# Kernel tuning notes

Hardware: AMD Instinct MI355X
Metric: run time of the kernel (lower is better)

## Reference

```python
import jax, jax.numpy as jnp
import numpy as np
from jax import lax

K = 3  # kernel_size
PAD = K // 2

def setup_inputs() -> dict:
    key = jax.random.key(0)
    ks = jax.random.split(key, 8)
    B, C, H, W = 8, 96, 128, 128
    x = jax.random.normal(ks[0], (B, C, H, W), dtype=jnp.float32)
    s = 0.05
    dw_w = jax.random.normal(ks[1], (C, 1, 3, 3), dtype=jnp.float32) * s   # depthwise 3x3
    dw_b = jax.random.normal(ks[2], (C,), dtype=jnp.float32) * s
    pw1_w = jax.random.normal(ks[3], (C // 2, C), dtype=jnp.float32) * s   # 1x1: C -> C/2
    pw1_b = jax.random.normal(ks[4], (C // 2,), dtype=jnp.float32) * s
    pw2_w = jax.random.normal(ks[5], (K * K, C // 2), dtype=jnp.float32) * s  # 1x1: C/2 -> 9
    pw2_b = jax.random.normal(ks[6], (K * K,), dtype=jnp.float32) * s
    return {"x": x, "dw_w": dw_w, "dw_b": dw_b, "pw1_w": pw1_w,
            "pw1_b": pw1_b, "pw2_w": pw2_w, "pw2_b": pw2_b}

def _unfold3x3(x):
    # x: (B,C,H,W) -> patches (B,C,9,H,W), index order (di*3+dj) matching F.unfold
    B, C, H, W = x.shape
    xp = jnp.pad(x, ((0, 0), (0, 0), (PAD, PAD), (PAD, PAD)))
    return jnp.stack([xp[:, :, i:i + H, j:j + W] for i in range(K) for j in range(K)], axis=2)

def _forward(x, dw_w, dw_b, pw1_w, pw1_b, pw2_w, pw2_b):
    B, C, H, W = x.shape
    # kernel predictor: depthwise 3x3 -> 1x1 -> leaky_relu(0.2) -> 1x1
    h = lax.conv_general_dilated(x, dw_w, (1, 1), ((PAD, PAD), (PAD, PAD)),
                                 dimension_numbers=("NCHW", "OIHW", "NCHW"),
                                 feature_group_count=C)
    h = h + dw_b[None, :, None, None]
    h = jnp.einsum("bchw,oc->bohw", h, pw1_w) + pw1_b[None, :, None, None]
    h = jnp.where(h >= 0, h, 0.2 * h)  # LeakyReLU(0.2)
    kw = jnp.einsum("bchw,oc->bohw", h, pw2_w) + pw2_b[None, :, None, None]  # (B,9,H,W)
    kw = jax.nn.softmax(kw, axis=1)
    patches = _unfold3x3(x)                      # (B,C,9,H,W)
    x_smooth = jnp.einsum("bckhw,bkhw->bchw", patches, kw)
    return x_smooth

def reference(x, dw_w, dw_b, pw1_w, pw1_b, pw2_w, pw2_b):
    return _forward(x, dw_w, dw_b, pw1_w, pw1_b, pw2_w, pw2_b)
```

## Files before the change

kernel.cpp:

```cpp
#include <hip/hip_runtime.h>
#include <math.h>

#define Cc 96
#define Hh 128
#define Ww 128
#define HWsz (Hh*Ww)
#define TW 16
#define TH 8
#define LROW 18
#define LPLANE 180
#define CPAD 104

typedef _Float16 h2 __attribute__((ext_vector_type(2)));
typedef short    s8v __attribute__((ext_vector_type(8)));
typedef float    f4v __attribute__((ext_vector_type(4)));

__device__ __forceinline__ unsigned pkrtz_u(float a, float b) {
    return __builtin_bit_cast(unsigned, __builtin_amdgcn_cvt_pkrtz(a, b));
}
__device__ __forceinline__ h2 pk2(float a, float b) {
    return __builtin_bit_cast(h2, __builtin_amdgcn_cvt_pkrtz(a, b));
}
__device__ __forceinline__ h2 u2h(unsigned u) { return __builtin_bit_cast(h2, u); }
__device__ __forceinline__ unsigned cvt_pk_bf16(float lo, float hi) {
    unsigned r;
    asm("v_cvt_pk_bf16_f32 %0, %1, %2" : "=v"(r) : "v"(lo), "v"(hi));
    return r;
}

__host__ __device__ __forceinline__ unsigned f2bf(float f) {
    unsigned u = __float_as_uint(f);
    return (u + 0x7fffu + ((u >> 16) & 1u)) >> 16;
}

#define GETW(v, wi) ((wi)==0 ? (v).x : (wi)==1 ? (v).y : (wi)==2 ? (v).z : (v).w)

#define OFF_WDW 0
#define OFF_W2  480
#define OFF_P1B 704
#define OFF_A   768
#define NPK     3072
#define WLDS_N  752

__global__ void alpf_prep(const float* __restrict__ dw_w, const float* __restrict__ dw_b,
                          const float* __restrict__ pw1_w, const float* __restrict__ pw1_b,
                          const float* __restrict__ pw2_w, unsigned* __restrict__ wpk)
{
    int i = blockIdx.x * 256 + threadIdx.x;
    if (i >= NPK) return;
    unsigned v = 0u;
    if (i < OFF_W2) {
        int g = i / 120, rem = i % 120, ks = rem / 40, s = rem % 40;
        int chb = 32*ks + 8*g;
        if (s < 4) v = pkrtz_u(dw_b[chb + 2*s], dw_b[chb + 2*s + 1]);
        else { int t = (s - 4) / 4, d = (s - 4) % 4;
               v = pkrtz_u(dw_w[(chb + 2*d)*9 + t], dw_w[(chb + 2*d + 1)*9 + t]); }
    } else if (i < OFF_P1B) {
        int idx = i - OFF_W2; int g = idx / 56, s = idx % 56;
        if (s < 54) { int k = s / 6, mm = s % 6, m = mm / 2, rp = mm % 2;
            int o = 16*m + 4*g + 2*rp;
            v = pkrtz_u(pw2_w[k*48 + o], pw2_w[k*48 + o + 1]); }
    } else if (i < OFF_P1B + 48) {
        v = __float_as_uint(pw1_b[i - OFF_P1B]);
    } else if (i >= OFF_A) {
        int idx = i - OFF_A; int f = idx / 256, rem = idx % 256, l = rem / 4, d = rem % 4;
        int m = f / 3, ks = f % 3;
        int o  = 16*m + (l & 15);
        int ch = 32*ks + 8*(l >> 4) + 2*d;
        v = f2bf(pw1_w[o*Cc + ch]) | (f2bf(pw1_w[o*Cc + ch + 1]) << 16);
    }
    wpk[i] = v;
}

__global__ __launch_bounds__(256, 4)
void alpf_fused(const float* __restrict__ x,
                const float* __restrict__ pw2_b,
                const unsigned* __restrict__ wpk,
                float* __restrict__ out)
{
    __shared__ unsigned short lx[LPLANE * CPAD];
    __shared__ unsigned wlds[WLDS_N];

    const int tid = threadIdx.x;

    const int nwg   = gridDim.x;
    const int chunk = nwg >> 3;
    const int logical = (blockIdx.x & 7) * chunk + (blockIdx.x >> 3);
    const int tx = logical & 7;
    const int ty = (logical >> 3) & 15;
    const int b  = logical >> 7;
    const int x0 = tx * TW;
    const int y0 = ty * TH;
    const float* __restrict__ xb = x + (size_t)b * Cc * HWsz;

    if (tid < 188)
        *reinterpret_cast<uint4*>(&wlds[tid * 4]) =
            *reinterpret_cast<const uint4*>(wpk + tid * 4);

    const int lane = tid & 63;
    const int g    = lane >> 4;
    const int c15  = lane & 15;
    const int wv   = tid >> 6;

    s8v Af[9];
    #pragma unroll
    for (int f = 0; f < 9; ++f)
        Af[f] = __builtin_bit_cast(s8v,
            *reinterpret_cast<const uint4*>(wpk + OFF_A + (f*64 + lane)*4));

    if (tid < LPLANE) {
        const int r1 = tid / LROW, q1 = tid - r1 * LROW;
        const int gy1 = y0 - 1 + r1, gx1 = x0 - 1 + q1;
        const bool ok1 = (gy1 >= 0) & (gy1 < Hh) & (gx1 >= 0) & (gx1 < Ww);
        const int g1 = gy1 * Ww + gx1;
        #pragma unroll 2
        for (int cg = 0; cg < 12; ++cg) {
            const int c0 = cg * 8;
            const float* xc = xb + (size_t)c0 * HWsz;
            float v0 = ok1 ? xc[0*HWsz + g1] : 0.f;
            float v1 = ok1 ? xc[1*HWsz + g1] : 0.f;
            float v2_ = ok1 ? xc[2*HWsz + g1] : 0.f;
            float v3 = ok1 ? xc[3*HWsz + g1] : 0.f;
            float v4 = ok1 ? xc[4*HWsz + g1] : 0.f;
            float v5 = ok1 ? xc[5*HWsz + g1] : 0.f;
            float v6 = ok1 ? xc[6*HWsz + g1] : 0.f;
            float v7 = ok1 ? xc[7*HWsz + g1] : 0.f;
            *reinterpret_cast<uint4*>(&lx[tid * CPAD + c0]) =
                make_uint4(pkrtz_u(v0,v1), pkrtz_u(v2_,v3), pkrtz_u(v4,v5), pkrtz_u(v6,v7));
        }
    }
    __syncthreads();

    f4v acc[3][2];
    #pragma unroll
    for (int m = 0; m < 3; ++m) {
        const f4v bb = *reinterpret_cast<const f4v*>(&wlds[OFF_P1B + 16*m + 4*g]);
        acc[m][0] = bb;
        acc[m][1] = bb;
    }

    #pragma unroll
    for (int ks = 0; ks < 3; ++ks) {
        const int base = (g*3 + ks) * 40;
        const uint4 wb = *reinterpret_cast<const uint4*>(&wlds[base]);
        uint4 wt[9];
        #pragma unroll
        for (int t = 0; t < 9; ++t)
            wt[t] = *reinterpret_cast<const uint4*>(&wlds[base + 4 + 4*t]);
        #pragma unroll
        for (int n = 0; n < 2; ++n) {
            h2 b0 = u2h(wb.x), b1 = u2h(wb.y), b2 = u2h(wb.z), b3 = u2h(wb.w);
            #pragma unroll
            for (int t = 0; t < 9; ++t) {
                const int dy = t / 3, dx = t - 3*dy;
                const uint4 xv = *reinterpret_cast<const uint4*>(
                    &lx[((2*wv + n + dy)*LROW + c15 + dx)*CPAD + 32*ks + 8*g]);
                b0 = __builtin_elementwise_fma(u2h(xv.x), u2h(wt[t].x), b0);
                b1 = __builtin_elementwise_fma(u2h(xv.y), u2h(wt[t].y), b1);
                b2 = __builtin_elementwise_fma(u2h(xv.z), u2h(wt[t].z), b2);
                b3 = __builtin_elementwise_fma(u2h(xv.w), u2h(wt[t].w), b3);
            }
            uint4 bq;
            bq.x = cvt_pk_bf16((float)b0.x, (float)b0.y);
            bq.y = cvt_pk_bf16((float)b1.x, (float)b1.y);
            bq.z = cvt_pk_bf16((float)b2.x, (float)b2.y);
            bq.w = cvt_pk_bf16((float)b3.x, (float)b3.y);
            const s8v Bf = __builtin_bit_cast(s8v, bq);
            acc[0][n] = __builtin_amdgcn_mfma_f32_16x16x32_bf16(Af[0 + ks], Bf, acc[0][n], 0, 0, 0);
            acc[1][n] = __builtin_amdgcn_mfma_f32_16x16x32_bf16(Af[3 + ks], Bf, acc[1][n], 0, 0, 0);
            acc[2][n] = __builtin_amdgcn_mfma_f32_16x16x32_bf16(Af[6 + ks], Bf, acc[2][n], 0, 0, 0);
        }
    }

    h2 tpk[2][3][2];
    #pragma unroll
    for (int n = 0; n < 2; ++n)
        #pragma unroll
        for (int m = 0; m < 3; ++m)
            #pragma unroll
            for (int rp = 0; rp < 2; ++rp) {
                float a = acc[m][n][2*rp], c = acc[m][n][2*rp + 1];
                a = (a >= 0.f) ? a : 0.2f * a;
                c = (c >= 0.f) ? c : 0.2f * c;
                tpk[n][m][rp] = pk2(a, c);
            }

    uint4 w2q[14];
    #pragma unroll
    for (int j = 0; j < 14; ++j)
        w2q[j] = *reinterpret_cast<const uint4*>(&wlds[OFF_W2 + g*56 + 4*j]);

    float kwr[2][9];
    #pragma unroll
    for (int k = 0; k < 9; ++k) {
        #pragma unroll
        for (int n = 0; n < 2; ++n) {
            h2 s = pk2(0.f, 0.f);
            #pragma unroll
            for (int m = 0; m < 3; ++m)
                #pragma unroll
                for (int rp = 0; rp < 2; ++rp) {
                    const int d = k*6 + 2*m + rp;
                    s = __builtin_elementwise_fma(tpk[n][m][rp],
                                                  u2h(GETW(w2q[d >> 2], d & 3)), s);
                }
            kwr[n][k] = (float)s.x + (float)s.y;
        }
    }
    #pragma unroll
    for (int n = 0; n < 2; ++n)
        #pragma unroll
        for (int k = 0; k < 9; ++k) {
            float v = kwr[n][k];
            v += __shfl_xor(v, 16);
            v += __shfl_xor(v, 32);
            kwr[n][k] = v + pw2_b[k];
        }

    const int nn  = (lane >> 4) & 1;
    const int chh = lane >> 5;
    const int row = 2*wv + nn;

    float kw[9];
    #pragma unroll
    for (int k = 0; k < 9; ++k) kw[k] = nn ? kwr[1][k] : kwr[0][k];

    float mx = kw[0];
    #pragma unroll
    for (int k = 1; k < 9; ++k) mx = fmaxf(mx, kw[k]);
    float sum = 0.f;
    #pragma unroll
    for (int k = 0; k < 9; ++k) { kw[k] = __expf(kw[k] - mx); sum += kw[k]; }
    const float inv = 1.f / sum;
    h2 kwp[9];
    #pragma unroll
    for (int k = 0; k < 9; ++k) { kw[k] *= inv; kwp[k] = pk2(kw[k], kw[k]); }

    const unsigned short* lb = &lx[(row * LROW + c15) * CPAD];
    float* __restrict__ ob = out + (size_t)b * Cc * HWsz + (size_t)(y0 + row) * Ww + (x0 + c15);
    #pragma unroll 2
    for (int cg = 0; cg < 6; ++cg) {
        const int c0 = chh * 48 + cg * 8;
        uint4 tp[9];
        #pragma unroll
        for (int k = 0; k < 9; ++k) {
            const int dy = k / 3, dx = k - 3 * dy;
            tp[k] = *reinterpret_cast<const uint4*>(&lb[(dy*LROW + dx)*CPAD + c0]);
        }
        #pragma unroll
        for (int l = 0; l < 4; ++l) {
            h2 a0 = u2h(GETW(tp[0], l)) * kwp[0];
            h2 a1 = u2h(GETW(tp[1], l)) * kwp[1];
            h2 a2 = u2h(GETW(tp[2], l)) * kwp[2];
            a0 = __builtin_elementwise_fma(u2h(GETW(tp[3], l)), kwp[3], a0);
            a1 = __builtin_elementwise_fma(u2h(GETW(tp[4], l)), kwp[4], a1);
            a2 = __builtin_elementwise_fma(u2h(GETW(tp[5], l)), kwp[5], a2);
            a0 = __builtin_elementwise_fma(u2h(GETW(tp[6], l)), kwp[6], a0);
            a1 = __builtin_elementwise_fma(u2h(GETW(tp[7], l)), kwp[7], a1);
            a2 = __builtin_elementwise_fma(u2h(GETW(tp[8], l)), kwp[8], a2);
            float olo = (float)a0.x + (float)a1.x + (float)a2.x;
            float ohi = (float)a0.y + (float)a1.y + (float)a2.y;
            ob[(size_t)(c0 + 2*l)     * HWsz] = olo;
            ob[(size_t)(c0 + 2*l + 1) * HWsz] = ohi;
        }
    }
}

extern "C" void kernel_launch(void* const* d_in, const int* in_sizes, int n_in,
                              void* d_out, int out_size, void* d_ws, size_t ws_size,
                              hipStream_t stream)
{
    const float* x     = (const float*)d_in[0];
    const float* dw_w  = (const float*)d_in[1];
    const float* dw_b  = (const float*)d_in[2];
    const float* pw1_w = (const float*)d_in[3];
    const float* pw1_b = (const float*)d_in[4];
    const float* pw2_w = (const float*)d_in[5];
    const float* pw2_b = (const float*)d_in[6];
    float* outp = (float*)d_out;
    unsigned* wpk = (unsigned*)d_ws;

    alpf_prep<<<(NPK + 255) / 256, 256, 0, stream>>>(dw_w, dw_b, pw1_w, pw1_b, pw2_w, wpk);

    const int B = in_sizes[0] / (Cc * HWsz);
    dim3 grid((Ww / TW) * (Hh / TH) * B);
    alpf_fused<<<grid, 256, 0, stream>>>(x, pw2_b, wpk, outp);
}
```

Baseline: 38.25 us.

## Vectorize halo tile staging with float4 loads and reuse LDS rows across output rows

Rewrites the global-to-LDS staging of the input tile. Each of the 256 threads now loads float4 row segments for channel pairs and writes packed halves, instead of 180 threads doing scalar per-pixel loads of 8 channels. The depthwise stage also preloads the 4x3 LDS neighbourhood into registers once per k-slice and shares it across the two output rows, which cuts redundant LDS reads. In exchange it uses more registers, and the LDS stores become 4-byte scattered writes that may cause bank conflicts.

Result: no change. 38.45 us (+0.5%).

```diff
diff --git a/kernel.cpp b/kernel.cpp
--- a/kernel.cpp
+++ b/kernel.cpp
@@ -108,26 +108,36 @@
         Af[f] = __builtin_bit_cast(s8v,
             *reinterpret_cast<const uint4*>(wpk + OFF_A + (f*64 + lane)*4));
 
-    if (tid < LPLANE) {
-        const int r1 = tid / LROW, q1 = tid - r1 * LROW;
-        const int gy1 = y0 - 1 + r1, gx1 = x0 - 1 + q1;
-        const bool ok1 = (gy1 >= 0) & (gy1 < Hh) & (gx1 >= 0) & (gx1 < Ww);
-        const int g1 = gy1 * Ww + gx1;
-        #pragma unroll 2
-        for (int cg = 0; cg < 12; ++cg) {
-            const int c0 = cg * 8;
-            const float* xc = xb + (size_t)c0 * HWsz;
-            float v0 = ok1 ? xc[0*HWsz + g1] : 0.f;
-            float v1 = ok1 ? xc[1*HWsz + g1] : 0.f;
-            float v2_ = ok1 ? xc[2*HWsz + g1] : 0.f;
-            float v3 = ok1 ? xc[3*HWsz + g1] : 0.f;
-            float v4 = ok1 ? xc[4*HWsz + g1] : 0.f;
-            float v5 = ok1 ? xc[5*HWsz + g1] : 0.f;
-            float v6 = ok1 ? xc[6*HWsz + g1] : 0.f;
-            float v7 = ok1 ? xc[7*HWsz + g1] : 0.f;
-            *reinterpret_cast<uint4*>(&lx[tid * CPAD + c0]) =
-                make_uint4(pkrtz_u(v0,v1), pkrtz_u(v2_,v3), pkrtz_u(v4,v5), pkrtz_u(v6,v7));
-        }
+    for (int t = tid; t < 960; t += 256) {
+        const int ri  = t / 96;
+        const int rem = t - ri * 96;
+        const int cp  = rem >> 1;
+        const int ph  = rem & 1;
+        const int gy  = y0 - 1 + ri;
+        const bool okr = (gy >= 0) & (gy < Hh);
+        const int gyc = okr ? gy : 0;
+        const int chA = 2 * cp;
+        const float* pA = xb + (size_t)chA * HWsz + gyc * Ww + x0 + 8 * ph;
+        const float* pB = pA + HWsz;
+        float4 a0 = *reinterpret_cast<const float4*>(pA);
+        float4 a1 = *reinterpret_cast<const float4*>(pA + 4);
+        float4 b0 = *reinterpret_cast<const float4*>(pB);
+        float4 b1 = *reinterpret_cast<const float4*>(pB + 4);
+        if (!okr) { a0 = make_float4(0,0,0,0); a1 = a0; b0 = a0; b1 = a0; }
+        const int ecol  = ph ? (x0 + 16) : (x0 - 1);
+        const bool oke  = okr & (ecol >= 0) & (ecol < Ww);
+        const int ecolc = (ecol >= 0 && ecol < Ww) ? ecol : 0;
+        const float* pE = xb + (size_t)chA * HWsz + gyc * Ww + ecolc;
+        float ea = pE[0], eb = pE[HWsz];
+        if (!oke) { ea = 0.f; eb = 0.f; }
+        const int prow = ri * LROW + 1 + 8 * ph;
+        #define STG(q, va, vb) \
+            *reinterpret_cast<unsigned*>(&lx[(prow + (q)) * CPAD + chA]) = pkrtz_u(va, vb)
+        STG(0, a0.x, b0.x); STG(1, a0.y, b0.y); STG(2, a0.z, b0.z); STG(3, a0.w, b0.w);
+        STG(4, a1.x, b1.x); STG(5, a1.y, b1.y); STG(6, a1.z, b1.z); STG(7, a1.w, b1.w);
+        #undef STG
+        const int eq = ri * LROW + (ph ? 17 : 0);
+        *reinterpret_cast<unsigned*>(&lx[eq * CPAD + chA]) = pkrtz_u(ea, eb);
     }
     __syncthreads();
 
@@ -147,14 +157,20 @@
         #pragma unroll
         for (int t = 0; t < 9; ++t)
             wt[t] = *reinterpret_cast<const uint4*>(&wlds[base + 4 + 4*t]);
+        uint4 xc_[4][3];
+        #pragma unroll
+        for (int r = 0; r < 4; ++r)
+            #pragma unroll
+            for (int d = 0; d < 3; ++d)
+                xc_[r][d] = *reinterpret_cast<const uint4*>(
+                    &lx[((2*wv + r)*LROW + c15 + d)*CPAD + 32*ks + 8*g]);
         #pragma unroll
         for (int n = 0; n < 2; ++n) {
             h2 b0 = u2h(wb.x), b1 = u2h(wb.y), b2 = u2h(wb.z), b3 = u2h(wb.w);
             #pragma unroll
             for (int t = 0; t < 9; ++t) {
                 const int dy = t / 3, dx = t - 3*dy;
-                const uint4 xv = *reinterpret_cast<const uint4*>(
-                    &lx[((2*wv + n + dy)*LROW + c15 + dx)*CPAD + 32*ks + 8*g]);
+                const uint4 xv = xc_[n + dy][dx];
                 b0 = __builtin_elementwise_fma(u2h(xv.x), u2h(wt[t].x), b0);
                 b1 = __builtin_elementwise_fma(u2h(xv.y), u2h(wt[t].y), b1);
                 b2 = __builtin_elementwise_fma(u2h(xv.z), u2h(wt[t].z), b2);
```
